# Performance work log

Hardware: AMD Instinct MI355X
Metric: run time of the kernel (lower is better)

Reference implementation:

```python
import jax, jax.numpy as jnp
import numpy as np


def setup_inputs() -> dict:
    key = jax.random.key(0)
    ks = jax.random.split(key, 7)
    B, IN, OUT, G = 8192, 2048, 2048, 4
    s_i = 1.0 / np.sqrt(IN)
    s_h = 1.0 / np.sqrt(OUT)
    return {
        "x": jax.random.normal(ks[0], (B, IN), jnp.float32),
        "prev_h": jax.random.normal(ks[1], (B, OUT), jnp.float32),
        "prev_c": jax.random.normal(ks[2], (B, OUT), jnp.float32),
        "Wi": jax.random.normal(ks[3], (G, IN, OUT), jnp.float32) * s_i,
        "Wh": jax.random.normal(ks[4], (G, OUT, OUT), jnp.float32) * s_h,
        "bi": jax.random.normal(ks[5], (G, OUT), jnp.float32) * s_i,
        "bh": jax.random.normal(ks[6], (G, OUT), jnp.float32) * s_h,
    }


def reference(x, prev_h, prev_c, Wi, Wh, bi, bh):
    # Two fused GEMMs replacing 8 per-gate Linears (gate order: in, forget, in2, out)
    # gates: [B, 4, OUT]
    gates = (jnp.einsum("bi,gio->bgo", x, Wi) + bi[None]
             + jnp.einsum("bh,gho->bgo", prev_h, Wh) + bh[None])
    in_gate = jax.nn.sigmoid(gates[:, 0])
    forget_gate = jax.nn.sigmoid(gates[:, 1])
    in_gate2 = jax.nn.sigmoid(gates[:, 2])
    out_gate = jax.nn.sigmoid(gates[:, 3])
    next_c = forget_gate * prev_c + in_gate * in_gate2
    # NOTE: faithful to source: out_gate + tanh(next_c) (addition, not multiply)
    next_h = out_gate + jnp.tanh(next_c)
    return next_h, next_c
```

## Files before the change

kernel.cpp:

```cpp
#include <hip/hip_runtime.h>
#include <stdint.h>


#define SZ_ELEMS 16777216
#define HALF_OUT 16777216

typedef __attribute__((ext_vector_type(8))) short bf16x8;
typedef __attribute__((ext_vector_type(4))) float f32x4;
typedef __attribute__((ext_vector_type(8))) unsigned short u16x8;

__device__ __forceinline__ unsigned short f2bf(float f) {
  unsigned int u = __float_as_uint(f);
  u += 0x7FFFu + ((u >> 16) & 1u);
  return (unsigned short)(u >> 16);
}

__device__ __forceinline__ void async16(const void* g, void* l) {
  __builtin_amdgcn_global_load_lds(
      (const __attribute__((address_space(1))) void*)g,
      (__attribute__((address_space(3))) void*)l, 16, 0, 0);
}

__device__ __forceinline__ float sigm(float x) { return 1.f / (1.f + __expf(-x)); }

__global__ void cvt_bf16_kernel(const float* __restrict__ src,
                                unsigned short* __restrict__ dst, int n4) {
  int i = blockIdx.x * blockDim.x + threadIdx.x;
  int stride = gridDim.x * blockDim.x;
  for (; i < n4; i += stride) {
    float4 v = reinterpret_cast<const float4*>(src)[i];
    ushort4 o;
    o.x = f2bf(v.x); o.y = f2bf(v.y); o.z = f2bf(v.z); o.w = f2bf(v.w);
    reinterpret_cast<ushort4*>(dst)[i] = o;
  }
}

__global__ void transpose_w_kernel(const float* __restrict__ Wi, const float* __restrict__ Wh,
                                   unsigned short* __restrict__ Wit, unsigned short* __restrict__ Wht) {
  __shared__ float tile[64][65];
  const int tk = blockIdx.x, to = blockIdx.y, gz = blockIdx.z;
  const float* W = (gz < 4 ? Wi : Wh) + (size_t)(gz & 3) * 4194304;
  unsigned short* Wt = (gz < 4 ? Wit : Wht) + (size_t)(gz & 3) * 4194304;
  const int t = threadIdx.x;
  const int o = t & 63, kr = t >> 6;
#pragma unroll
  for (int p = 0; p < 16; ++p) {
    int k = p * 4 + kr;
    tile[k][o] = W[(size_t)(tk * 64 + k) * 2048 + to * 64 + o];
  }
  __syncthreads();
#pragma unroll
  for (int p = 0; p < 2; ++p) {
    int idx = p * 256 + t;
    int orow = idx >> 3, k0 = (idx & 7) * 8;
    u16x8 v;
#pragma unroll
    for (int i = 0; i < 8; ++i) v[i] = f2bf(tile[k0 + i][orow]);
    *reinterpret_cast<u16x8*>(&Wt[(size_t)(to * 64 + orow) * 2048 + tk * 64 + k0]) = v;
  }
}

#define FENCE asm volatile("" ::: "memory")
#define BARRIER do { FENCE; __builtin_amdgcn_s_barrier(); FENCE; } while (0)
#define VMC6  asm volatile("s_waitcnt vmcnt(6)" ::: "memory")
#define VMC4  asm volatile("s_waitcnt vmcnt(4)" ::: "memory")
#define VMC0  asm volatile("s_waitcnt vmcnt(0)" ::: "memory")

__global__ __launch_bounds__(512, 2) void lstm_gemm_kernel(
    const unsigned short* __restrict__ xb, const unsigned short* __restrict__ hb,
    const unsigned short* __restrict__ wit, const unsigned short* __restrict__ wht,
    const float* __restrict__ bi, const float* __restrict__ bh,
    const float* __restrict__ prev_c, float* __restrict__ out) {
  __shared__ char lds[131072];

  const int tid = threadIdx.x;
  const int wave = tid >> 6, lane = tid & 63;
  const int wm = wave >> 2, wn = wave & 3;
  const int bm = blockIdx.x;
  const int bo = blockIdx.y;

  const int kwin = (lane >> 4) << 4;
  const int fswz = (lane & 7) << 4;
  int aro[8], bro[4];
#pragma unroll
  for (int mf = 0; mf < 8; ++mf) aro[mf] = (wm * 128 + mf * 16 + (lane & 15)) * 128;
#pragma unroll
  for (int nf = 0; nf < 4; ++nf) bro[nf] = 32768 + (nf * 64 + wn * 16 + (lane & 15)) * 128;

  const int L0 = tid * 16;
  int agoff[2][2], bgoff[2][2];
#pragma unroll
  for (int h = 0; h < 2; ++h)
#pragma unroll
    for (int j = 0; j < 2; ++j) {
      int L = j * 8192 + L0;
      int row = h * 128 + (L >> 7);
      int c = (L & 127) ^ ((row & 7) << 4);
      agoff[h][j] = row * 4096 + c;
      int g = row >> 6, orow = row & 63;
      bgoff[h][j] = g * 8388608 + orow * 4096 + c;
    }
  const char* pxa = (const char*)xb + (size_t)bm * 1048576;
  const char* pha = (const char*)hb + (size_t)bm * 1048576;
  const char* pwi = (const char*)wit + (size_t)bo * 262144;
  const char* pwh = (const char*)wht + (size_t)bo * 262144;

  auto stageA = [&](int t, int h, int buf) {
    const char* base = (t < 32) ? (pxa + t * 128) : (pha + (t - 32) * 128);
    char* d = lds + buf * 65536 + h * 16384 + L0;
    async16(base + agoff[h][0], d);
    async16(base + agoff[h][1], d + 8192);
  };
  auto stageB = [&](int t, int h, int buf) {
    const char* base = (t < 32) ? (pwi + t * 128) : (pwh + (t - 32) * 128);
    char* d = lds + buf * 65536 + 32768 + h * 16384 + L0;
    async16(base + bgoff[h][0], d);
    async16(base + bgoff[h][1], d + 8192);
  };

  f32x4 acc[8][4];
  const f32x4 zero = {0.f, 0.f, 0.f, 0.f};
#pragma unroll
  for (int mf = 0; mf < 8; ++mf)
#pragma unroll
    for (int nf = 0; nf < 4; ++nf) acc[mf][nf] = zero;

  bf16x8 afrA[4][2];
  bf16x8 afrB[4][2];
  bf16x8 bfr[4][2];

  auto loadAA = [&](int buf) {
    const char* l = lds + buf * 65536;
#pragma unroll
    for (int m = 0; m < 4; ++m)
#pragma unroll
      for (int ks = 0; ks < 2; ++ks)
        afrA[m][ks] = *(const bf16x8*)(l + aro[m] + ((ks * 64 + kwin) ^ fswz));
  };
  auto loadAB = [&](int buf) {
    const char* l = lds + buf * 65536;
#pragma unroll
    for (int m = 0; m < 4; ++m)
#pragma unroll
      for (int ks = 0; ks < 2; ++ks)
        afrB[m][ks] = *(const bf16x8*)(l + aro[4 + m] + ((ks * 64 + kwin) ^ fswz));
  };
  auto loadB0 = [&](int buf) {
    const char* l = lds + buf * 65536;
#pragma unroll
    for (int n = 0; n < 2; ++n)
#pragma unroll
      for (int ks = 0; ks < 2; ++ks)
        bfr[n][ks] = *(const bf16x8*)(l + bro[n] + ((ks * 64 + kwin) ^ fswz));
  };
  auto loadB1 = [&](int buf) {
    const char* l = lds + buf * 65536;
#pragma unroll
    for (int n = 0; n < 2; ++n)
#pragma unroll
      for (int ks = 0; ks < 2; ++ks)
        bfr[2 + n][ks] = *(const bf16x8*)(l + bro[2 + n] + ((ks * 64 + kwin) ^ fswz));
  };
  auto MQ = [&](int mh, int nh) {
    __builtin_amdgcn_s_setprio(1);
#pragma unroll
    for (int ks = 0; ks < 2; ++ks)
#pragma unroll
      for (int n = 0; n < 2; ++n)
#pragma unroll
        for (int m = 0; m < 4; ++m)
          acc[mh * 4 + m][nh * 2 + n] = __builtin_amdgcn_mfma_f32_16x16x32_bf16(
              (mh ? afrB : afrA)[m][ks], bfr[nh * 2 + n][ks],
              acc[mh * 4 + m][nh * 2 + n], 0, 0, 0);
    __builtin_amdgcn_s_setprio(0);
  };

  stageB(0, 0, 0); stageB(0, 1, 0); stageA(0, 0, 0); stageA(0, 1, 0);
  stageB(1, 0, 1); stageB(1, 1, 1); stageA(1, 0, 1);
  VMC6;
  BARRIER;
  loadAA(0); loadB0(0);

  for (int i = 0; i < 31; ++i) {
    const int t1 = 2 * i + 1, t2 = 2 * i + 2, t3 = 2 * i + 3;
    stageA(t1, 1, 1); MQ(0, 0); loadB1(0); BARRIER;
    stageB(t2, 0, 0); MQ(0, 1); loadAB(0); BARRIER;
    stageB(t2, 1, 0); MQ(1, 0); VMC4; BARRIER;
    stageA(t2, 0, 0); MQ(1, 1); loadAA(1); loadB0(1); BARRIER;
    stageA(t2, 1, 0); MQ(0, 0); loadB1(1); BARRIER;
    stageB(t3, 0, 1); MQ(0, 1); loadAB(1); BARRIER;
    stageB(t3, 1, 1); MQ(1, 0); VMC4; BARRIER;
    stageA(t3, 0, 1); MQ(1, 1); loadAA(0); loadB0(0); BARRIER;
  }

  stageA(63, 1, 1); MQ(0, 0); loadB1(0); BARRIER;
  MQ(0, 1); loadAB(0); BARRIER;
  MQ(1, 0); VMC0; BARRIER;
  MQ(1, 1); loadAA(1); loadB0(1); BARRIER;
  MQ(0, 0); loadB1(1); BARRIER;
  MQ(0, 1); loadAB(1); BARRIER;
  MQ(1, 0); BARRIER;
  MQ(1, 1);

  const int col = lane & 15, rg = lane >> 4;
  const int o = bo * 64 + wn * 16 + col;
  float bs[4];
#pragma unroll
  for (int g = 0; g < 4; ++g) bs[g] = bi[g * 2048 + o] + bh[g * 2048 + o];
#pragma unroll
  for (int mf = 0; mf < 8; ++mf) {
    int bbase = bm * 256 + wm * 128 + mf * 16 + rg * 4;
#pragma unroll
    for (int r = 0; r < 4; ++r) {
      int b = bbase + r;
      float gi = sigm(acc[mf][0][r] + bs[0]);
      float gf = sigm(acc[mf][1][r] + bs[1]);
      float g2 = sigm(acc[mf][2][r] + bs[2]);
      float go = sigm(acc[mf][3][r] + bs[3]);
      float c = prev_c[(size_t)b * 2048 + o];
      float nc = gf * c + gi * g2;
      float e = __expf(2.f * nc);
      float nh = go + (e - 1.f) / (e + 1.f);
      out[(size_t)b * 2048 + o] = nh;
      out[(size_t)HALF_OUT + (size_t)b * 2048 + o] = nc;
    }
  }
}

extern "C" void kernel_launch(void* const* d_in, const int* in_sizes, int n_in,
                              void* d_out, int out_size, void* d_ws, size_t ws_size,
                              hipStream_t stream) {
  const float* x  = (const float*)d_in[0];
  const float* ph = (const float*)d_in[1];
  const float* pc = (const float*)d_in[2];
  const float* Wi = (const float*)d_in[3];
  const float* Wh = (const float*)d_in[4];
  const float* bi = (const float*)d_in[5];
  const float* bh = (const float*)d_in[6];
  float* out = (float*)d_out;

  if (ws_size < (size_t)4 * SZ_ELEMS * sizeof(unsigned short)) return;
  unsigned short* xb  = (unsigned short*)d_ws;
  unsigned short* hb  = xb + SZ_ELEMS;
  unsigned short* wit = hb + SZ_ELEMS;
  unsigned short* wht = wit + SZ_ELEMS;

  cvt_bf16_kernel<<<2048, 256, 0, stream>>>(x, xb, 4194304);
  cvt_bf16_kernel<<<2048, 256, 0, stream>>>(ph, hb, 4194304);
  transpose_w_kernel<<<dim3(32, 32, 8), 256, 0, stream>>>(Wi, Wh, wit, wht);
  lstm_gemm_kernel<<<dim3(32, 32), 512, 0, stream>>>(xb, hb, wit, wht, bi, bh, pc, out);
}
```

Baseline: 510.7 us.

## Load weight fragments directly from global memory instead of staging through LDS

The B (weight) operand tiles are no longer staged into LDS. Each wave now loads its bf16 weight fragments straight from global memory into registers, and the schedule is reworked around this. LDS use drops from 128KB to 64KB and the waitcnt thresholds change. This removes LDS write/read traffic for B and frees shared memory. The cost is that the four waves in a row each fetch the same weight data, which raises global/L2 traffic, and global-load latency is now exposed to the MFMA loop with less explicit prefetch distance.

```diff
diff --git a/kernel.cpp b/kernel.cpp
--- a/kernel.cpp
+++ b/kernel.cpp
@@ -62,8 +62,7 @@
 
 #define FENCE asm volatile("" ::: "memory")
 #define BARRIER do { FENCE; __builtin_amdgcn_s_barrier(); FENCE; } while (0)
-#define VMC6  asm volatile("s_waitcnt vmcnt(6)" ::: "memory")
-#define VMC4  asm volatile("s_waitcnt vmcnt(4)" ::: "memory")
+#define VMC2  asm volatile("s_waitcnt vmcnt(2)" ::: "memory")
 #define VMC0  asm volatile("s_waitcnt vmcnt(0)" ::: "memory")
 
 __global__ __launch_bounds__(512, 2) void lstm_gemm_kernel(
@@ -71,7 +70,7 @@
     const unsigned short* __restrict__ wit, const unsigned short* __restrict__ wht,
     const float* __restrict__ bi, const float* __restrict__ bh,
     const float* __restrict__ prev_c, float* __restrict__ out) {
-  __shared__ char lds[131072];
+  __shared__ char lds[65536];
 
   const int tid = threadIdx.x;
   const int wave = tid >> 6, lane = tid & 63;
@@ -81,24 +80,26 @@
 
   const int kwin = (lane >> 4) << 4;
   const int fswz = (lane & 7) << 4;
-  int aro[8], bro[4];
+  int aro[8];
 #pragma unroll
   for (int mf = 0; mf < 8; ++mf) aro[mf] = (wm * 128 + mf * 16 + (lane & 15)) * 128;
-#pragma unroll
-  for (int nf = 0; nf < 4; ++nf) bro[nf] = 32768 + (nf * 64 + wn * 16 + (lane & 15)) * 128;
+
+  int bgo[4][2];
+#pragma unroll
+  for (int nf = 0; nf < 4; ++nf)
+#pragma unroll
+    for (int ks = 0; ks < 2; ++ks)
+      bgo[nf][ks] = nf * 8388608 + (wn * 16 + (lane & 15)) * 4096 + ks * 64 + kwin;
 
   const int L0 = tid * 16;
-  int agoff[2][2], bgoff[2][2];
+  int agoff[2][2];
 #pragma unroll
   for (int h = 0; h < 2; ++h)
 #pragma unroll
     for (int j = 0; j < 2; ++j) {
       int L = j * 8192 + L0;
       int row = h * 128 + (L >> 7);
-      int c = (L & 127) ^ ((row & 7) << 4);
-      agoff[h][j] = row * 4096 + c;
-      int g = row >> 6, orow = row & 63;
-      bgoff[h][j] = g * 8388608 + orow * 4096 + c;
+      agoff[h][j] = row * 4096 + ((L & 127) ^ ((row & 7) << 4));
     }
   const char* pxa = (const char*)xb + (size_t)bm * 1048576;
   const char* pha = (const char*)hb + (size_t)bm * 1048576;
@@ -107,15 +108,9 @@
 
   auto stageA = [&](int t, int h, int buf) {
     const char* base = (t < 32) ? (pxa + t * 128) : (pha + (t - 32) * 128);
-    char* d = lds + buf * 65536 + h * 16384 + L0;
+    char* d = lds + buf * 32768 + h * 16384 + L0;
     async16(base + agoff[h][0], d);
     async16(base + agoff[h][1], d + 8192);
-  };
-  auto stageB = [&](int t, int h, int buf) {
-    const char* base = (t < 32) ? (pwi + t * 128) : (pwh + (t - 32) * 128);
-    char* d = lds + buf * 65536 + 32768 + h * 16384 + L0;
-    async16(base + bgoff[h][0], d);
-    async16(base + bgoff[h][1], d + 8192);
   };
 
   f32x4 acc[8][4];
@@ -130,7 +125,7 @@
   bf16x8 bfr[4][2];
 
   auto loadAA = [&](int buf) {
-    const char* l = lds + buf * 65536;
+    const char* l = lds + buf * 32768;
 #pragma unroll
     for (int m = 0; m < 4; ++m)
 #pragma unroll
@@ -138,28 +133,28 @@
         afrA[m][ks] = *(const bf16x8*)(l + aro[m] + ((ks * 64 + kwin) ^ fswz));
   };
   auto loadAB = [&](int buf) {
-    const char* l = lds + buf * 65536;
+    const char* l = lds + buf * 32768;
 #pragma unroll
     for (int m = 0; m < 4; ++m)
 #pragma unroll
       for (int ks = 0; ks < 2; ++ks)
         afrB[m][ks] = *(const bf16x8*)(l + aro[4 + m] + ((ks * 64 + kwin) ^ fswz));
   };
-  auto loadB0 = [&](int buf) {
-    const char* l = lds + buf * 65536;
+  auto loadB0G = [&](int t) {
+    const char* base = (t < 32) ? (pwi + t * 128) : (pwh + (t - 32) * 128);
 #pragma unroll
     for (int n = 0; n < 2; ++n)
 #pragma unroll
       for (int ks = 0; ks < 2; ++ks)
-        bfr[n][ks] = *(const bf16x8*)(l + bro[n] + ((ks * 64 + kwin) ^ fswz));
-  };
-  auto loadB1 = [&](int buf) {
-    const char* l = lds + buf * 65536;
+        bfr[n][ks] = *(const bf16x8*)(base + bgo[n][ks]);
+  };
+  auto loadB1G = [&](int t) {
+    const char* base = (t < 32) ? (pwi + t * 128) : (pwh + (t - 32) * 128);
 #pragma unroll
     for (int n = 0; n < 2; ++n)
 #pragma unroll
       for (int ks = 0; ks < 2; ++ks)
-        bfr[2 + n][ks] = *(const bf16x8*)(l + bro[2 + n] + ((ks * 64 + kwin) ^ fswz));
+        bfr[2 + n][ks] = *(const bf16x8*)(base + bgo[2 + n][ks]);
   };
   auto MQ = [&](int mh, int nh) {
     __builtin_amdgcn_s_setprio(1);
@@ -175,31 +170,30 @@
     __builtin_amdgcn_s_setprio(0);
   };
 
-  stageB(0, 0, 0); stageB(0, 1, 0); stageA(0, 0, 0); stageA(0, 1, 0);
-  stageB(1, 0, 1); stageB(1, 1, 1); stageA(1, 0, 1);
-  VMC6;
+  stageA(0, 0, 0); stageA(0, 1, 0); stageA(1, 0, 1);
+  VMC2;
   BARRIER;
-  loadAA(0); loadB0(0);
+  loadAA(0); loadB0G(0);
 
   for (int i = 0; i < 31; ++i) {
-    const int t1 = 2 * i + 1, t2 = 2 * i + 2, t3 = 2 * i + 3;
-    stageA(t1, 1, 1); MQ(0, 0); loadB1(0); BARRIER;
-    stageB(t2, 0, 0); MQ(0, 1); loadAB(0); BARRIER;
-    stageB(t2, 1, 0); MQ(1, 0); VMC4; BARRIER;
-    stageA(t2, 0, 0); MQ(1, 1); loadAA(1); loadB0(1); BARRIER;
-    stageA(t2, 1, 0); MQ(0, 0); loadB1(1); BARRIER;
-    stageB(t3, 0, 1); MQ(0, 1); loadAB(1); BARRIER;
-    stageB(t3, 1, 1); MQ(1, 0); VMC4; BARRIER;
-    stageA(t3, 0, 1); MQ(1, 1); loadAA(0); loadB0(0); BARRIER;
-  }
-
-  stageA(63, 1, 1); MQ(0, 0); loadB1(0); BARRIER;
+    const int t0 = 2 * i, t1 = 2 * i + 1, t2 = 2 * i + 2, t3 = 2 * i + 3;
+    loadB1G(t0); stageA(t1, 1, 1); MQ(0, 0); BARRIER;
+    MQ(0, 1); loadAB(0); BARRIER;
+    stageA(t2, 0, 0); MQ(1, 0); VMC2; BARRIER;
+    MQ(1, 1); loadAA(1); loadB0G(t1); BARRIER;
+    loadB1G(t1); stageA(t2, 1, 0); MQ(0, 0); BARRIER;
+    MQ(0, 1); loadAB(1); BARRIER;
+    stageA(t3, 0, 1); MQ(1, 0); VMC2; BARRIER;
+    MQ(1, 1); loadAA(0); loadB0G(t2); BARRIER;
+  }
+
+  loadB1G(62); stageA(63, 1, 1); MQ(0, 0); BARRIER;
   MQ(0, 1); loadAB(0); BARRIER;
   MQ(1, 0); VMC0; BARRIER;
-  MQ(1, 1); loadAA(1); loadB0(1); BARRIER;
-  MQ(0, 0); loadB1(1); BARRIER;
+  MQ(1, 1); loadAA(1); loadB0G(63); BARRIER;
+  loadB1G(63); MQ(0, 0); BARRIER;
   MQ(0, 1); loadAB(1); BARRIER;
-  MQ(1, 0); BARRIER;
+  MQ(1, 0);
   MQ(1, 1);
 
   const int col = lane & 15, rg = lane >> 4;
```

Result: slower. 907.2 us (+77.6%).
